# Kernel tuning notes

Hardware: AMD Instinct MI355X
Metric: run time of the kernel (lower is better)

## Reference

```python
import jax, jax.numpy as jnp
import numpy as np

ND, NT, B = 16384, 16384, 4096
FD, FT, C = 256, 256, 768


def _gat(x_src, x_dst, ei, Ws, Wd, a_s, a_d, b, num_dst, self_loops):
    """PyG GATConv, heads=1: per-edge attention softmax over incoming edges."""
    if self_loops:
        loops = jnp.arange(num_dst, dtype=ei.dtype)
        ei = jnp.concatenate([ei, jnp.stack([loops, loops])], axis=1)
    src, dst = ei[0], ei[1]
    hs = x_src @ Ws                                   # [Ns, C]
    hd = x_dst @ Wd                                   # [Ndst, C]
    e = jax.nn.leaky_relu((hs @ a_s)[src] + (hd @ a_d)[dst], 0.2)   # [E]
    m = jax.ops.segment_max(e, dst, num_segments=num_dst)
    p = jnp.exp(e - m[dst])
    s = jax.ops.segment_sum(p, dst, num_segments=num_dst)
    alpha = p / (s[dst] + 1e-16)
    out = jax.ops.segment_sum(hs[src] * alpha[:, None], dst, num_segments=num_dst)
    return out + b


def _l2norm(x):
    n = jnp.linalg.norm(x, axis=1, keepdims=True)
    return x / jnp.maximum(n, 1e-12)


def setup_inputs() -> dict:
    ks = iter(jax.random.split(jax.random.key(0), 64))
    def nrm(shape, fan_in=None):
        s = 1.0 if fan_in is None else (1.0 / fan_in) ** 0.5
        return jax.random.normal(next(ks), shape, jnp.float32) * s
    inp = {}
    inp["x_drug"] = nrm((ND, FD))
    inp["x_target"] = nrm((NT, FT))
    inp["cell_features"] = nrm((B, 890))
    for et, fs, fd in (("dd", FD, FD), ("dt", FD, FT), ("tt", FT, FT)):
        inp[f"W_src_{et}"] = nrm((fs, C), fs)
        inp[f"W_dst_{et}"] = nrm((fd, C), fd)
        inp[f"a_src_{et}"] = nrm((C,), C)
        inp[f"a_dst_{et}"] = nrm((C,), C)
        inp[f"b_{et}"] = jnp.zeros((C,), jnp.float32)
    for name, fi, fo in (("red1", 890, 2048), ("red2", 2048, 512), ("red3", 512, 2 * C),
                         ("r2a", 4 * C, 2048), ("r2b", 2048, 512), ("r2c", 512, C), ("cls", C, 2)):
        inp[f"{name}_w"] = nrm((fi, fo), fi)
        inp[f"{name}_b"] = jnp.zeros((fo,), jnp.float32)
    inp["drug1_id"] = jax.random.randint(next(ks), (B,), 0, ND)
    inp["drug2_id"] = jax.random.randint(next(ks), (B,), 0, ND)
    inp["ei_dd"] = jax.random.randint(next(ks), (2, 131072), 0, ND)
    inp["ei_dt"] = jnp.stack([jax.random.randint(next(ks), (262144,), 0, ND),
                              jax.random.randint(next(ks), (262144,), 0, NT)])
    inp["ei_tt"] = jax.random.randint(next(ks), (2, 262144), 0, NT)
    return inp


def reference(x_drug, x_target, cell_features,
              W_src_dd, W_dst_dd, a_src_dd, a_dst_dd, b_dd,
              W_src_dt, W_dst_dt, a_src_dt, a_dst_dt, b_dt,
              W_src_tt, W_dst_tt, a_src_tt, a_dst_tt, b_tt,
              red1_w, red1_b, red2_w, red2_b, red3_w, red3_b,
              r2a_w, r2a_b, r2b_w, r2b_b, r2c_w, r2c_b,
              cls_w, cls_b,
              drug1_id, drug2_id, ei_dd, ei_dt, ei_tt):
    # HeteroConv (aggr='sum') followed by per-type ReLU, num_layers=1
    drug = jax.nn.relu(_gat(x_drug, x_drug, ei_dd,
                            W_src_dd, W_dst_dd, a_src_dd, a_dst_dd, b_dd, ND, True))
    target = jax.nn.relu(
        _gat(x_drug, x_target, ei_dt, W_src_dt, W_dst_dt, a_src_dt, a_dst_dt, b_dt, NT, False)
        + _gat(x_target, x_target, ei_tt, W_src_tt, W_dst_tt, a_src_tt, a_dst_tt, b_tt, NT, True))
    del target  # with num_layers=1 the target embeddings never feed the output (faithful)
    d1 = drug[drug1_id]
    d2 = drug[drug2_id]
    cell = _l2norm(cell_features)
    cell = jax.nn.relu(cell @ red1_w + red1_b)
    cell = jax.nn.relu(cell @ red2_w + red2_b)
    cell = jax.nn.relu(cell @ red3_w + red3_b)          # [B, 2*C]
    hidden = _l2norm(jnp.concatenate([d1, d2, cell], axis=1))  # [B, 4*C]
    hidden = jax.nn.relu(hidden @ r2a_w + r2a_b)
    hidden = jax.nn.relu(hidden @ r2b_w + r2b_b)
    hidden = jax.nn.relu(hidden @ r2c_w + r2c_b)
    return hidden @ cls_w + cls_b                       # [B, 2]
```

## Files before the change

### kernel.cpp

```cpp
#include <hip/hip_runtime.h>
#include <cstdint>

#define ND 16384
#define BATCH 4096
#define CDIM 768
#define E_DD 131072
#define FD 256

typedef unsigned short u16;
typedef u16 u16x4 __attribute__((ext_vector_type(4)));
typedef u16 u16x8 __attribute__((ext_vector_type(8)));
typedef short s16x8 __attribute__((ext_vector_type(8)));
typedef float f32x4 __attribute__((ext_vector_type(4)));

__device__ __forceinline__ u16 f2bf(float x) {
  union { float f; uint32_t u; } v; v.f = x;
  uint32_t r = v.u + 0x7fffu + ((v.u >> 16) & 1u);
  return (u16)(r >> 16);
}
__device__ __forceinline__ float bf2f(u16 h) {
  union { float f; uint32_t u; } v; v.u = ((uint32_t)h) << 16;
  return v.f;
}
__device__ __forceinline__ uint32_t split2p(float x) {
  u16 h = f2bf(x);
  u16 l = f2bf(x - bf2f(h));
  return ((uint32_t)h << 16) | l;
}

#define GLOAD_LDS16(gp, lp)                                                   \
  __builtin_amdgcn_global_load_lds(                                           \
      (__attribute__((address_space(1))) void*)(gp),                          \
      (__attribute__((address_space(3))) void*)(lp), 16, 0, 0)

#define KP 40

template <int KS, int OUT_BF16, int RELU, int BIAS, int ASPLIT, int ALO, int BLO,
          int BKD>
__device__ __forceinline__ void gemm_core(
    int bx, int by, int bz,
    const float* __restrict__ Af,
    const u16* __restrict__ Ahi, const u16* __restrict__ Alo,
    const u16* __restrict__ Bhi, const u16* __restrict__ Blo,
    const float* __restrict__ bias,
    float* __restrict__ Cf, u16* __restrict__ Chi,
    int M, int N, int K, u16* AsB, u16* BsB) {
  constexpr int MT = 4, NT = 4;
  constexpr int BM = 128, BN = 128;
  constexpr int ASEG = BM / 64;
  constexpr int BSEG = BN / 64;
  constexpr bool DIRECT = (ASPLIT == 0 && ALO == 0 && BLO == 0);

  const int t = threadIdx.x;
  const int bm0 = bx * BM, bn0 = by * BN;
  const int wid = t >> 6, lane = t & 63;
  const int quad = lane >> 4, l16 = lane & 15;
  const int wm0 = (wid >> 1) * (MT * 16);
  const int wn0 = (wid & 1) * (NT * 16);

  const int chunk = K / KS;
  const int kbeg = (KS > 1) ? bz * chunk : 0;
  const int kend = kbeg + chunk;

  float bvv[NT];
#pragma unroll
  for (int ni = 0; ni < NT; ++ni)
    bvv[ni] = BIAS ? bias[bn0 + wn0 + ni * 16 + l16] : 0.f;

  f32x4 acc[MT][NT];
#pragma unroll
  for (int i = 0; i < MT; ++i)
#pragma unroll
    for (int j = 0; j < NT; ++j) acc[i][j] = (f32x4){0.f, 0.f, 0.f, 0.f};

  if constexpr (DIRECT) {
    constexpr int SLOTS = BKD / 8;
    constexpr int SM = SLOTS - 1;
    constexpr int NLD = (BM * BKD) / (256 * 8);
    auto stageA = [&](int buf, int kk) {
#pragma unroll
      for (int c = 0; c < NLD; ++c) {
        int s = t + 256 * c;
        int r = s / SLOTS, j = s % SLOTS;
        int jj = j ^ (r & SM);
        size_t goff = (size_t)(bm0 + r) * K + kk + jj * 8;
        int lofs = __builtin_amdgcn_readfirstlane((wid * 64 + 256 * c) * 8);
        GLOAD_LDS16(Ahi + goff, AsB + buf * (BM * BKD) + lofs);
      }
    };
    auto stageB = [&](int buf, int kk) {
#pragma unroll
      for (int c = 0; c < NLD; ++c) {
        int s = t + 256 * c;
        int r = s / SLOTS, j = s % SLOTS;
        int jj = j ^ (r & SM);
        size_t goff = (size_t)(bn0 + r) * K + kk + jj * 8;
        int lofs = __builtin_amdgcn_readfirstlane((wid * 64 + 256 * c) * 8);
        GLOAD_LDS16(Bhi + goff, BsB + buf * (BN * BKD) + lofs);
      }
    };
    const int rsw = l16 & SM;
    stageA(0, kbeg);
    stageB(0, kbeg);
    int cur = 0;
    for (int k0 = kbeg;;) {
      __syncthreads();
      int kn = k0 + BKD;
      if (kn < kend) {
        stageA(cur ^ 1, kn);
        stageB(cur ^ 1, kn);
      }
      const u16* Ab = AsB + cur * (BM * BKD);
      const u16* Bb = BsB + cur * (BN * BKD);
#pragma unroll
      for (int h = 0; h < BKD / 32; ++h) {
        s16x8 ah[MT], bh[NT];
#pragma unroll
        for (int mi = 0; mi < MT; ++mi)
          ah[mi] = *(const s16x8*)(Ab + (wm0 + mi * 16 + l16) * BKD +
                                   (((h * 4 + quad) ^ rsw) * 8));
#pragma unroll
        for (int ni = 0; ni < NT; ++ni)
          bh[ni] = *(const s16x8*)(Bb + (wn0 + ni * 16 + l16) * BKD +
                                   (((h * 4 + quad) ^ rsw) * 8));
#pragma unroll
        for (int mi = 0; mi < MT; ++mi)
#pragma unroll
          for (int ni = 0; ni < NT; ++ni)
            acc[mi][ni] = __builtin_amdgcn_mfma_f32_16x16x32_bf16(
                ah[mi], bh[ni], acc[mi][ni], 0, 0, 0);
      }
      k0 = kn;
      cur ^= 1;
      if (k0 >= kend) break;
    }
  } else {
    auto As = [&](int a, int r, int k) -> u16& { return AsB[(a * BM + r) * KP + k]; };
    auto Bs = [&](int a, int r, int k) -> u16& { return BsB[(a * BN + r) * KP + k]; };

    u16x8 pAh[ASEG], pAl[ASEG], pBh[BSEG], pBl[BSEG];

    auto loadA = [&](int c, int kk) {
      int s = t + 256 * c, row = s >> 2, kq = (s & 3) * 8;
      size_t off = (size_t)(bm0 + row) * K + kk + kq;
      if (ASPLIT) {
        f32x4 v0 = *(const f32x4*)(Af + off);
        f32x4 v1 = *(const f32x4*)(Af + off + 4);
        u16x8 h, l;
#pragma unroll
        for (int e = 0; e < 4; ++e) {
          uint32_t p = split2p(v0[e]);
          h[e] = (u16)(p >> 16); l[e] = (u16)(p & 0xffffu);
          uint32_t q = split2p(v1[e]);
          h[e + 4] = (u16)(q >> 16); l[e + 4] = (u16)(q & 0xffffu);
        }
        pAh[c] = h; pAl[c] = l;
      } else {
        pAh[c] = *(const u16x8*)(Ahi + off);
        if (ALO) pAl[c] = *(const u16x8*)(Alo + off);
      }
    };
    auto loadB = [&](int c, int kk) {
      int s = t + 256 * c, row = s >> 2, kq = (s & 3) * 8;
      size_t off = (size_t)(bn0 + row) * K + kk + kq;
      pBh[c] = *(const u16x8*)(Bhi + off);
      if (BLO) pBl[c] = *(const u16x8*)(Blo + off);
    };

#pragma unroll
    for (int c = 0; c < ASEG; ++c) loadA(c, kbeg);
#pragma unroll
    for (int c = 0; c < BSEG; ++c) loadB(c, kbeg);

    for (int k0 = kbeg;;) {
      __syncthreads();
#pragma unroll
      for (int c = 0; c < ASEG; ++c) {
        int s = t + 256 * c, row = s >> 2, kq = (s & 3) * 8;
        *(u16x8*)&As(0, row, kq) = pAh[c];
        if (ALO) *(u16x8*)&As(1, row, kq) = pAl[c];
      }
#pragma unroll
      for (int c = 0; c < BSEG; ++c) {
        int s = t + 256 * c, row = s >> 2, kq = (s & 3) * 8;
        *(u16x8*)&Bs(0, row, kq) = pBh[c];
        if (BLO) *(u16x8*)&Bs(1, row, kq) = pBl[c];
      }
      __syncthreads();

      int kn = k0 + 32;
      if (kn < kend) {
#pragma unroll
        for (int c = 0; c < ASEG; ++c) loadA(c, kn);
#pragma unroll
        for (int c = 0; c < BSEG; ++c) loadB(c, kn);
      }

      s16x8 ah[MT], al[MT], bh[NT], bl[NT];
#pragma unroll
      for (int mi = 0; mi < MT; ++mi) {
        ah[mi] = *(const s16x8*)&As(0, wm0 + mi * 16 + l16, quad * 8);
        if (ALO) al[mi] = *(const s16x8*)&As(1, wm0 + mi * 16 + l16, quad * 8);
      }
#pragma unroll
      for (int ni = 0; ni < NT; ++ni) {
        bh[ni] = *(const s16x8*)&Bs(0, wn0 + ni * 16 + l16, quad * 8);
        if (BLO) bl[ni] = *(const s16x8*)&Bs(1, wn0 + ni * 16 + l16, quad * 8);
      }
#pragma unroll
      for (int mi = 0; mi < MT; ++mi)
#pragma unroll
        for (int ni = 0; ni < NT; ++ni) {
          acc[mi][ni] = __builtin_amdgcn_mfma_f32_16x16x32_bf16(
              ah[mi], bh[ni], acc[mi][ni], 0, 0, 0);
          if (BLO)
            acc[mi][ni] = __builtin_amdgcn_mfma_f32_16x16x32_bf16(
                ah[mi], bl[ni], acc[mi][ni], 0, 0, 0);
          if (ALO)
            acc[mi][ni] = __builtin_amdgcn_mfma_f32_16x16x32_bf16(
                al[mi], bh[ni], acc[mi][ni], 0, 0, 0);
        }
      k0 = kn;
      if (k0 >= kend) break;
    }
  }

  float* Cp = (KS > 1) ? Cf + (size_t)bz * M * N : Cf;
#pragma unroll
  for (int mi = 0; mi < MT; ++mi) {
#pragma unroll
    for (int ni = 0; ni < NT; ++ni) {
      int row = bm0 + wm0 + mi * 16 + quad * 4;
      int col = bn0 + wn0 + ni * 16 + l16;
#pragma unroll
      for (int r = 0; r < 4; ++r) {
        float v = acc[mi][ni][r] + bvv[ni];
        if (RELU) v = fmaxf(v, 0.f);
        size_t o = (size_t)(row + r) * N + col;
        if (OUT_BF16) Chi[o] = f2bf(v);
        else Cp[o] = v;
      }
    }
  }
}

template <int KS, int OUT_BF16, int RELU, int BIAS, int ASPLIT, int ALO, int BLO,
          int BKD>
__global__ __launch_bounds__(256) void mfma_gemm(
    const float* __restrict__ Af,
    const u16* __restrict__ Ahi, const u16* __restrict__ Alo,
    const u16* __restrict__ Bhi, const u16* __restrict__ Blo,
    const float* __restrict__ bias,
    float* __restrict__ Cf, u16* __restrict__ Chi,
    int M, int N, int K) {
  constexpr bool DIRECT = (ASPLIT == 0 && ALO == 0 && BLO == 0);
  __shared__ __align__(16) u16 AsB[DIRECT ? 2 * 128 * BKD : (ALO ? 2 : 1) * 128 * KP];
  __shared__ __align__(16) u16 BsB[DIRECT ? 2 * 128 * BKD : (BLO ? 2 : 1) * 128 * KP];
  gemm_core<KS, OUT_BF16, RELU, BIAS, ASPLIT, ALO, BLO, BKD>(
      blockIdx.x, blockIdx.y, (KS > 1) ? (int)blockIdx.z : 0,
      Af, Ahi, Alo, Bhi, Blo, bias, Cf, Chi, M, N, K, AsB, BsB);
}

__device__ __forceinline__ void gat_body(
    int idx, int t,
    const u16* __restrict__ hs, const float* __restrict__ es,
    const float* __restrict__ ed, const int* __restrict__ offsets,
    const int* __restrict__ slots, const float* __restrict__ bias,
    const int* __restrict__ list, const int* __restrict__ cnt,
    u16* __restrict__ out) {
  if (idx >= *cnt) return;
  int d = list[idx];
  int lane = t & 63;
  int beg = offsets[d], end = offsets[d + 1];
  float edv = ed[d];
  float mx = -1e30f;
  for (int j = beg + lane; j < end; j += 64) {
    float e = es[slots[j]] + edv;
    e = e >= 0.f ? e : 0.2f * e;
    mx = fmaxf(mx, e);
  }
#pragma unroll
  for (int m = 32; m; m >>= 1) mx = fmaxf(mx, __shfl_xor(mx, m));
  float sm = 0.f;
  for (int j = beg + lane; j < end; j += 64) {
    float e = es[slots[j]] + edv;
    e = e >= 0.f ? e : 0.2f * e;
    sm += expf(e - mx);
  }
#pragma unroll
  for (int m = 32; m; m >>= 1) sm += __shfl_xor(sm, m);
  float inv = 1.f / (sm + 1e-16f);
  int c8 = lane * 8;
  int c4 = 512 + lane * 4;
  float a8[8] = {};
  float a4[4] = {};
  for (int j = beg; j < end; ++j) {
    int srcn = slots[j];
    float e = es[srcn] + edv;
    e = e >= 0.f ? e : 0.2f * e;
    float alpha = expf(e - mx) * inv;
    const u16* hrow = hs + (size_t)srcn * CDIM;
    u16x8 r8 = *(const u16x8*)(hrow + c8);
    u16x4 r4 = *(const u16x4*)(hrow + c4);
#pragma unroll
    for (int e2 = 0; e2 < 8; ++e2) a8[e2] = fmaf(alpha, bf2f(r8[e2]), a8[e2]);
#pragma unroll
    for (int e2 = 0; e2 < 4; ++e2) a4[e2] = fmaf(alpha, bf2f(r4[e2]), a4[e2]);
  }
  u16* orow = out + (size_t)d * CDIM;
  u16x8 o8;
  u16x4 o4;
#pragma unroll
  for (int e2 = 0; e2 < 8; ++e2) o8[e2] = f2bf(fmaxf(a8[e2] + bias[c8 + e2], 0.f));
#pragma unroll
  for (int e2 = 0; e2 < 4; ++e2) o4[e2] = f2bf(fmaxf(a4[e2] + bias[c4 + e2], 0.f));
  *(u16x8*)(orow + c8) = o8;
  *(u16x4*)(orow + c4) = o4;
}

__global__ __launch_bounds__(256) void dual_gemm_red1_hs_scatter(
    const u16* __restrict__ cn, const u16* __restrict__ r1T,
    const float* __restrict__ red1_b, u16* __restrict__ c1,
    const float* __restrict__ xd, const u16* __restrict__ wsrcT,
    u16* __restrict__ hs,
    const int* __restrict__ src, const int* __restrict__ dst,
    int* __restrict__ cursor, int* __restrict__ slots) {
  __shared__ __align__(16) u16 SMEM[16384];
  int b = blockIdx.x;
  if (b < 512) {
    gemm_core<1, 1, 1, 1, 0, 0, 0, 32>(b & 31, b >> 5, 0, nullptr, cn, nullptr,
                                       r1T, nullptr, red1_b, nullptr, c1,
                                       BATCH, 2048, 896, SMEM, SMEM + 2 * 128 * 32);
  } else if (b < 1280) {
    int b2 = b - 512;
    gemm_core<1, 1, 0, 0, 1, 1, 0, 32>(b2 & 127, b2 >> 7, 0, xd, nullptr, nullptr,
                                       wsrcT, nullptr, nullptr, nullptr, hs,
                                       ND, CDIM, FD, SMEM, SMEM + 2 * 128 * KP);
  } else {
    int e = (b - 1280) * 256 + threadIdx.x;
    if (e < E_DD) {
      int pos = atomicAdd(&cursor[dst[e]], 1);
      slots[pos] = src[e];
    }
  }
}

__global__ __launch_bounds__(256) void red2_gat(
    const u16* __restrict__ c1, const u16* __restrict__ r2T,
    float* __restrict__ P,
    const u16* __restrict__ hs, const float* __restrict__ es,
    const float* __restrict__ ed, const int* __restrict__ offsets,
    const int* __restrict__ slots, const float* __restrict__ bias,
    const int* __restrict__ list, const int* __restrict__ cnt,
    u16* __restrict__ drug) {
  __shared__ __align__(16) u16 SMEM[16384];
  int b = blockIdx.x;
  if (b < 512) {
    gemm_core<4, 0, 0, 0, 0, 0, 0, 32>(b & 31, (b >> 5) & 3, b >> 7,
                                       nullptr, c1, nullptr, r2T, nullptr,
                                       nullptr, P, nullptr,
                                       BATCH, 512, 2048, SMEM, SMEM + 2 * 128 * 32);
  } else {
    gat_body((b - 512) * 4 + (threadIdx.x >> 6), threadIdx.x,
             hs, es, ed, offsets, slots, bias, list, cnt, drug);
  }
}

template <int KS>
__global__ void reduce_split_ks(const float* __restrict__ P,
                                const float* __restrict__ bias,
                                u16* __restrict__ Chi, int M, int N) {
  int i = blockIdx.x * 256 + threadIdx.x;
  int total = (M * N) >> 2;
  if (i >= total) return;
  f32x4 s = ((const f32x4*)P)[i];
#pragma unroll
  for (int z = 1; z < KS; ++z) s += ((const f32x4*)P)[(size_t)z * total + i];
  int col = (i * 4) % N;
  f32x4 bv = *(const f32x4*)(bias + col);
  u16x4 h;
#pragma unroll
  for (int e = 0; e < 4; ++e) h[e] = f2bf(fmaxf(s[e] + bv[e], 0.f));
  *(u16x4*)&Chi[i * 4] = h;
}

__global__ void reduce_cls(const float* __restrict__ P,
                           const float* __restrict__ bias,
                           const float* __restrict__ clsw,
                           const float* __restrict__ clsb,
                           float* __restrict__ out) {
  int row = blockIdx.x * 4 + (threadIdx.x >> 6);
  int lane = threadIdx.x & 63;
  const f32x4* p0 = (const f32x4*)(P + (size_t)row * CDIM);
  const f32x4* p1 = (const f32x4*)(P + (size_t)BATCH * CDIM + (size_t)row * CDIM);
  float s0 = 0.f, s1 = 0.f;
#pragma unroll
  for (int i = 0; i < 3; ++i) {
    int c4 = lane + 64 * i;
    f32x4 a = p0[c4] + p1[c4];
    f32x4 bv = *(const f32x4*)(bias + c4 * 4);
#pragma unroll
    for (int e = 0; e < 4; ++e) {
      float h = fmaxf(a[e] + bv[e], 0.f);
      int c = c4 * 4 + e;
      s0 = fmaf(h, clsw[c * 2 + 0], s0);
      s1 = fmaf(h, clsw[c * 2 + 1], s1);
    }
  }
#pragma unroll
  for (int m = 32; m; m >>= 1) {
    s0 += __shfl_xor(s0, m);
    s1 += __shfl_xor(s1, m);
  }
  if (lane == 0) {
    out[row * 2 + 0] = s0 + clsb[0];
    out[row * 2 + 1] = s1 + clsb[1];
  }
}

struct TDesc {
  const float* W;
  u16* Th;
  int K, N, Kpad, start;
};
struct TPack { TDesc d[7]; };

#define P1_T 11328
#define P1_W (P1_T + 256)
#define P1_I (P1_W + 64)
__global__ __launch_bounds__(256) void prep1(
    TPack p,
    const float* __restrict__ Wsrc, const float* __restrict__ Wdst,
    const float* __restrict__ a_s, const float* __restrict__ a_d,
    float* __restrict__ wsv, float* __restrict__ wdv,
    int* __restrict__ counts, int* __restrict__ mask, int* __restrict__ cnt,
    const float* __restrict__ cellf, u16* __restrict__ cn_hi) {
  __shared__ __align__(16) float S[1088];
  int b = blockIdx.x;
  int t = threadIdx.x;
  if (b < P1_T) {
    float (*tile)[33] = (float(*)[33])S;
    int mi = 0;
#pragma unroll
    for (int i = 1; i < 7; ++i)
      if (b >= p.d[i].start) mi = i;
    TDesc dd = p.d[mi];
    int rel = b - dd.start;
    int tilesX = dd.Kpad / 32;
    int k0 = (rel % tilesX) * 32, n0 = (rel / tilesX) * 32;
    int tx = t & 31, ty = t >> 5;
#pragma unroll
    for (int i = 0; i < 4; ++i) {
      int k = k0 + ty + 8 * i, n = n0 + tx;
      tile[ty + 8 * i][tx] = (k < dd.K && n < dd.N) ? dd.W[(size_t)k * dd.N + n] : 0.f;
    }
    __syncthreads();
#pragma unroll
    for (int i = 0; i < 4; ++i) {
      int n = n0 + ty + 8 * i, k = k0 + tx;
      if (n < dd.N) dd.Th[(size_t)n * dd.Kpad + k] = f2bf(tile[tx][ty + 8 * i]);
    }
  } else if (b < P1_W) {
    int k = b - P1_T;
    float* rs = S;
    float* rd = S + 256;
    float s = 0.f, d = 0.f;
    for (int c = t; c < CDIM; c += 256) {
      s += Wsrc[(size_t)k * CDIM + c] * a_s[c];
      d += Wdst[(size_t)k * CDIM + c] * a_d[c];
    }
    rs[t] = s; rd[t] = d;
    __syncthreads();
    for (int st = 128; st; st >>= 1) {
      if (t < st) { rs[t] += rs[t + st]; rd[t] += rd[t + st]; }
      __syncthreads();
    }
    if (t == 0) { wsv[k] = rs[0]; wdv[k] = rd[0]; }
  } else if (b < P1_I) {
    int i = (b - P1_W) * 256 + t;
    if (i < ND) { counts[i] = 1; mask[i] = 0; }
    if (i == 0) *cnt = 0;
  } else {
    int row = b - P1_I;
    float* red = S;
    const float* irow = cellf + (size_t)row * 890;
    float s = 0.f;
    for (int c = t; c < 890; c += 256) { float v = irow[c]; s += v * v; }
    red[t] = s;
    __syncthreads();
    for (int st = 128; st; st >>= 1) {
      if (t < st) red[t] += red[t + st];
      __syncthreads();
    }
    float inv = 1.f / fmaxf(sqrtf(red[0]), 1e-12f);
    for (int c = t; c < 896; c += 256) {
      float v = (c < 890) ? irow[c] * inv : 0.f;
      cn_hi[(size_t)row * 896 + c] = f2bf(v);
    }
  }
}

#define P2_E (ND * FD / 1024)
#define P2_M (P2_E + BATCH / 256)
__global__ __launch_bounds__(256) void prep2(
    const float* __restrict__ x, const float* __restrict__ wsv,
    const float* __restrict__ wdv, float* __restrict__ es, float* __restrict__ ed,
    const int* __restrict__ d1, const int* __restrict__ d2, int* __restrict__ mask,
    const int* __restrict__ dst, int* __restrict__ counts) {
  int b = blockIdx.x, t = threadIdx.x;
  if (b < P2_E) {
    int i = b * 256 + t;
    int lane = t & 63;
    int row = i >> 6;
    int c4 = lane * 4;
    f32x4 v = ((const f32x4*)x)[i];
    f32x4 ws = *(const f32x4*)(wsv + c4);
    f32x4 wd = *(const f32x4*)(wdv + c4);
    float a = v[0] * ws[0] + v[1] * ws[1] + v[2] * ws[2] + v[3] * ws[3];
    float bb = v[0] * wd[0] + v[1] * wd[1] + v[2] * wd[2] + v[3] * wd[3];
#pragma unroll
    for (int m = 32; m; m >>= 1) {
      a += __shfl_xor(a, m);
      bb += __shfl_xor(bb, m);
    }
    if (lane == 0) { es[row] = a; ed[row] = bb; }
  } else if (b < P2_M) {
    int i = (b - P2_E) * 256 + t;
    mask[d1[i]] = 1;
    mask[d2[i]] = 1;
  } else {
    int e = (b - P2_M) * 256 + t;
    atomicAdd(&counts[dst[e]], 1);
  }
}

__global__ __launch_bounds__(512) void prep3(
    const int* __restrict__ mask, int* __restrict__ cnt, int* __restrict__ list,
    const int* __restrict__ counts, int* __restrict__ offsets,
    int* __restrict__ cursor, int* __restrict__ slots) {
  __shared__ int part[512];
  int b = blockIdx.x, t = threadIdx.x;
  if (b < 32) {
    int i = b * 512 + t;
    if (mask[i]) {
      int pos = atomicAdd(cnt, 1);
      list[pos] = i;
    }
  } else {
    int base = t * 32;
    int s = 0;
    for (int i = 0; i < 32; ++i) s += counts[base + i];
    part[t] = s;
    __syncthreads();
    if (t == 0) {
      int run = 0;
      for (int i = 0; i < 512; ++i) { int tmp = part[i]; part[i] = run; run += tmp; }
      offsets[ND] = run;
    }
    __syncthreads();
    int run = part[t];
    for (int i = 0; i < 32; ++i) {
      int d = base + i;
      offsets[d] = run;
      slots[run] = d;
      cursor[d] = run + 1;
      run += counts[d];
    }
  }
}

__global__ __launch_bounds__(256) void hidden_build_bf16(
    const u16* __restrict__ drug, const u16* __restrict__ c3,
    const int* __restrict__ d1, const int* __restrict__ d2,
    u16* __restrict__ hhi) {
  int row = blockIdx.x;
  int t = threadIdx.x;
  const u16* s1 = drug + (size_t)d1[row] * CDIM;
  const u16* s2 = drug + (size_t)d2[row] * CDIM;
  const u16* s3 = c3 + (size_t)row * (2 * CDIM);
  float vals[12];
  float ss = 0.f;
#pragma unroll
  for (int i = 0; i < 12; ++i) {
    int c = t + 256 * i;
    float v;
    if (i < 3)      v = bf2f(s1[c]);
    else if (i < 6) v = bf2f(s2[c - CDIM]);
    else            v = bf2f(s3[c - 2 * CDIM]);
    vals[i] = v;
    ss += v * v;
  }
  __shared__ float red[256];
  red[t] = ss;
  __syncthreads();
  for (int st = 128; st; st >>= 1) {
    if (t < st) red[t] += red[t + st];
    __syncthreads();
  }
  float inv = 1.f / fmaxf(sqrtf(red[0]), 1e-12f);
  u16* hrow_h = hhi + (size_t)row * (4 * CDIM);
#pragma unroll
  for (int i = 0; i < 12; ++i) hrow_h[t + 256 * i] = f2bf(vals[i] * inv);
}

extern "C" void kernel_launch(void* const* d_in, const int* in_sizes, int n_in,
                              void* d_out, int out_size, void* d_ws, size_t ws_size,
                              hipStream_t stream) {
  const float* x_drug   = (const float*)d_in[0];
  const float* cellf    = (const float*)d_in[2];
  const float* W_src_dd = (const float*)d_in[3];
  const float* W_dst_dd = (const float*)d_in[4];
  const float* a_src_dd = (const float*)d_in[5];
  const float* a_dst_dd = (const float*)d_in[6];
  const float* b_dd     = (const float*)d_in[7];
  const float* red1_w = (const float*)d_in[18];
  const float* red1_b = (const float*)d_in[19];
  const float* red2_w = (const float*)d_in[20];
  const float* red2_b = (const float*)d_in[21];
  const float* red3_w = (const float*)d_in[22];
  const float* red3_b = (const float*)d_in[23];
  const float* r2a_w  = (const float*)d_in[24];
  const float* r2a_b  = (const float*)d_in[25];
  const float* r2b_w  = (const float*)d_in[26];
  const float* r2b_b  = (const float*)d_in[27];
  const float* r2c_w  = (const float*)d_in[28];
  const float* r2c_b  = (const float*)d_in[29];
  const float* cls_w  = (const float*)d_in[30];
  const float* cls_b  = (const float*)d_in[31];
  const int* drug1_id = (const int*)d_in[32];
  const int* drug2_id = (const int*)d_in[33];
  const int* ei_dd    = (const int*)d_in[34];
  float* out = (float*)d_out;

  const int* dd_src = ei_dd;
  const int* dd_dst = ei_dd + E_DD;

  char* w = (char*)d_ws;
  size_t off = 0;
  auto alloc = [&](size_t bytes) -> char* {
    char* p = w + off;
    off = (off + bytes + 255) & ~(size_t)255;
    return p;
  };
  u16* hs   = (u16*)alloc((size_t)ND * CDIM * 2);
  u16* drug = (u16*)alloc((size_t)ND * CDIM * 2);
  u16* c3   = (u16*)alloc((size_t)BATCH * 2 * CDIM * 2);
  float* P  = (float*)alloc((size_t)4 * BATCH * 512 * 4);
  u16* hid_hi = hs;
  u16* cn_hi = (u16*)alloc((size_t)BATCH * 896 * 2);
  u16* c1_hi = (u16*)alloc((size_t)BATCH * 2048 * 2);
  u16* c2_hi = (u16*)alloc((size_t)BATCH * 512 * 2);
  u16* wsrcT_hi = (u16*)alloc((size_t)CDIM * FD * 2);
  u16* r1T_hi = (u16*)alloc((size_t)2048 * 896 * 2);
  u16* r2T_hi = (u16*)alloc((size_t)512 * 2048 * 2);
  u16* r3T_hi = (u16*)alloc((size_t)1536 * 512 * 2);
  u16* raT_hi = (u16*)alloc((size_t)2048 * 3072 * 2);
  u16* rbT_hi = (u16*)alloc((size_t)512 * 2048 * 2);
  u16* rcT_hi = (u16*)alloc((size_t)768 * 512 * 2);
  float* es  = (float*)alloc((size_t)ND * 4);
  float* ed  = (float*)alloc((size_t)ND * 4);
  float* wsv = (float*)alloc(FD * 4);
  float* wdv = (float*)alloc(FD * 4);
  int* counts  = (int*)alloc((size_t)ND * 4);
  int* offsets = (int*)alloc((size_t)(ND + 1) * 4);
  int* cursor  = (int*)alloc((size_t)ND * 4);
  int* slots   = (int*)alloc((size_t)(E_DD + ND) * 4);
  int* mask    = (int*)alloc((size_t)ND * 4);
  int* list    = (int*)alloc((size_t)ND * 4);
  int* cnt     = (int*)alloc(256);
  (void)ws_size; (void)n_in; (void)in_sizes; (void)out_size;

  TPack tp;
  tp.d[0] = {W_src_dd, wsrcT_hi, 256, 768, 256, 0};
  tp.d[1] = {red1_w, r1T_hi, 890, 2048, 896, 192};
  tp.d[2] = {red2_w, r2T_hi, 2048, 512, 2048, 1984};
  tp.d[3] = {red3_w, r3T_hi, 512, 1536, 512, 3008};
  tp.d[4] = {r2a_w, raT_hi, 3072, 2048, 3072, 3776};
  tp.d[5] = {r2b_w, rbT_hi, 2048, 512, 2048, 9920};
  tp.d[6] = {r2c_w, rcT_hi, 512, 768, 512, 10944};
  prep1<<<15744, 256, 0, stream>>>(tp, W_src_dd, W_dst_dd, a_src_dd, a_dst_dd,
                                   wsv, wdv, counts, mask, cnt, cellf, cn_hi);

  prep2<<<4624, 256, 0, stream>>>(x_drug, wsv, wdv, es, ed, drug1_id, drug2_id,
                                  mask, dd_dst, counts);

  prep3<<<33, 512, 0, stream>>>(mask, cnt, list, counts, offsets, cursor, slots);

  dual_gemm_red1_hs_scatter<<<1792, 256, 0, stream>>>(
      cn_hi, r1T_hi, red1_b, c1_hi, x_drug, wsrcT_hi, hs,
      dd_src, dd_dst, cursor, slots);

  red2_gat<<<4608, 256, 0, stream>>>(c1_hi, r2T_hi, P,
                                     hs, es, ed, offsets, slots, b_dd, list,
                                     cnt, drug);
  reduce_split_ks<4><<<BATCH * 512 / 1024, 256, 0, stream>>>(P, red2_b, c2_hi, BATCH, 512);
  mfma_gemm<1, 1, 1, 1, 0, 0, 0, 64><<<dim3(BATCH / 128, 1536 / 128), 256, 0, stream>>>(
      nullptr, c2_hi, nullptr, r3T_hi, nullptr, red3_b, nullptr, c3, BATCH, 1536, 512);

  hidden_build_bf16<<<BATCH, 256, 0, stream>>>(drug, c3, drug1_id, drug2_id, hid_hi);

  mfma_gemm<1, 1, 1, 1, 0, 0, 0, 64><<<dim3(BATCH / 128, 2048 / 128), 256, 0, stream>>>(
      nullptr, hid_hi, nullptr, raT_hi, nullptr, r2a_b, nullptr, c1_hi, BATCH, 2048, 3072);
  mfma_gemm<4, 0, 0, 0, 0, 0, 0, 64><<<dim3(BATCH / 128, 512 / 128, 4), 256, 0, stream>>>(
      nullptr, c1_hi, nullptr, rbT_hi, nullptr, nullptr, P, nullptr, BATCH, 512, 2048);
  reduce_split_ks<4><<<BATCH * 512 / 1024, 256, 0, stream>>>(P, r2b_b, c2_hi, BATCH, 512);
  mfma_gemm<2, 0, 0, 0, 0, 0, 0, 64><<<dim3(BATCH / 128, CDIM / 128, 2), 256, 0, stream>>>(
      nullptr, c2_hi, nullptr, rcT_hi, nullptr, nullptr, P, nullptr, BATCH, CDIM, 512);
  reduce_cls<<<BATCH / 4, 256, 0, stream>>>(P, r2c_b, cls_w, cls_b, out);
}
```

Before: 445.0 us.

## Remap GEMM workgroups per XCD and split red2 GEMM from GAT aggregation

Result: no change. 452.3 us (+1.6%).

```diff
diff --git a/kernel.cpp b/kernel.cpp
--- a/kernel.cpp
+++ b/kernel.cpp
@@ -32,6 +32,12 @@
   __builtin_amdgcn_global_load_lds(                                           \
       (__attribute__((address_space(1))) void*)(gp),                          \
       (__attribute__((address_space(3))) void*)(lp), 16, 0, 0)
+
+__device__ __forceinline__ int xcd_chunk(int f, int nwg) {
+  int q = nwg >> 3, r = nwg & 7;
+  int xcd = f & 7, s = f >> 3;
+  return (xcd < r ? xcd * (q + 1) : r * (q + 1) + (xcd - r) * q) + s;
+}
 
 #define KP 40
 
@@ -256,8 +262,11 @@
   constexpr bool DIRECT = (ASPLIT == 0 && ALO == 0 && BLO == 0);
   __shared__ __align__(16) u16 AsB[DIRECT ? 2 * 128 * BKD : (ALO ? 2 : 1) * 128 * KP];
   __shared__ __align__(16) u16 BsB[DIRECT ? 2 * 128 * BKD : (BLO ? 2 : 1) * 128 * KP];
+  int f = blockIdx.x + gridDim.x * blockIdx.y;
+  int wg = xcd_chunk(f, gridDim.x * gridDim.y);
+  int bx = wg % gridDim.x, by = wg / gridDim.x;
   gemm_core<KS, OUT_BF16, RELU, BIAS, ASPLIT, ALO, BLO, BKD>(
-      blockIdx.x, blockIdx.y, (KS > 1) ? (int)blockIdx.z : 0,
+      bx, by, (KS > 1) ? (int)blockIdx.z : 0,
       Af, Ahi, Alo, Bhi, Blo, bias, Cf, Chi, M, N, K, AsB, BsB);
 }
 
@@ -318,6 +327,16 @@
   *(u16x4*)(orow + c4) = o4;
 }
 
+__global__ __launch_bounds__(256) void gat_aggregate(
+    const u16* __restrict__ hs, const float* __restrict__ es,
+    const float* __restrict__ ed, const int* __restrict__ offsets,
+    const int* __restrict__ slots, const float* __restrict__ bias,
+    const int* __restrict__ list, const int* __restrict__ cnt,
+    u16* __restrict__ out) {
+  gat_body(blockIdx.x * 4 + (threadIdx.x >> 6), threadIdx.x,
+           hs, es, ed, offsets, slots, bias, list, cnt, out);
+}
+
 __global__ __launch_bounds__(256) void dual_gemm_red1_hs_scatter(
     const u16* __restrict__ cn, const u16* __restrict__ r1T,
     const float* __restrict__ red1_b, u16* __restrict__ c1,
@@ -328,7 +347,8 @@
   __shared__ __align__(16) u16 SMEM[16384];
   int b = blockIdx.x;
   if (b < 512) {
-    gemm_core<1, 1, 1, 1, 0, 0, 0, 32>(b & 31, b >> 5, 0, nullptr, cn, nullptr,
+    int wg = xcd_chunk(b, 512);
+    gemm_core<1, 1, 1, 1, 0, 0, 0, 32>(wg & 31, wg >> 5, 0, nullptr, cn, nullptr,
                                        r1T, nullptr, red1_b, nullptr, c1,
                                        BATCH, 2048, 896, SMEM, SMEM + 2 * 128 * 32);
   } else if (b < 1280) {
@@ -342,27 +362,6 @@
       int pos = atomicAdd(&cursor[dst[e]], 1);
       slots[pos] = src[e];
     }
-  }
-}
-
-__global__ __launch_bounds__(256) void red2_gat(
-    const u16* __restrict__ c1, const u16* __restrict__ r2T,
-    float* __restrict__ P,
-    const u16* __restrict__ hs, const float* __restrict__ es,
-    const float* __restrict__ ed, const int* __restrict__ offsets,
-    const int* __restrict__ slots, const float* __restrict__ bias,
-    const int* __restrict__ list, const int* __restrict__ cnt,
-    u16* __restrict__ drug) {
-  __shared__ __align__(16) u16 SMEM[16384];
-  int b = blockIdx.x;
-  if (b < 512) {
-    gemm_core<4, 0, 0, 0, 0, 0, 0, 32>(b & 31, (b >> 5) & 3, b >> 7,
-                                       nullptr, c1, nullptr, r2T, nullptr,
-                                       nullptr, P, nullptr,
-                                       BATCH, 512, 2048, SMEM, SMEM + 2 * 128 * 32);
-  } else {
-    gat_body((b - 512) * 4 + (threadIdx.x >> 6), threadIdx.x,
-             hs, es, ed, offsets, slots, bias, list, cnt, drug);
   }
 }
 
@@ -690,12 +689,13 @@
       cn_hi, r1T_hi, red1_b, c1_hi, x_drug, wsrcT_hi, hs,
       dd_src, dd_dst, cursor, slots);
 
-  red2_gat<<<4608, 256, 0, stream>>>(c1_hi, r2T_hi, P,
-                                     hs, es, ed, offsets, slots, b_dd, list,
-                                     cnt, drug);
+  mfma_gemm<4, 0, 0, 0, 0, 0, 0, 64><<<dim3(BATCH / 128, 512 / 128, 4), 256, 0, stream>>>(
+      nullptr, c1_hi, nullptr, r2T_hi, nullptr, nullptr, P, nullptr, BATCH, 512, 2048);
   reduce_split_ks<4><<<BATCH * 512 / 1024, 256, 0, stream>>>(P, red2_b, c2_hi, BATCH, 512);
   mfma_gemm<1, 1, 1, 1, 0, 0, 0, 64><<<dim3(BATCH / 128, 1536 / 128), 256, 0, stream>>>(
       nullptr, c2_hi, nullptr, r3T_hi, nullptr, red3_b, nullptr, c3, BATCH, 1536, 512);
+
+  gat_aggregate<<<ND / 4, 256, 0, stream>>>(hs, es, ed, offsets, slots, b_dd, list, cnt, drug);
 
   hidden_build_bf16<<<BATCH, 256, 0, stream>>>(drug, c3, drug1_id, drug2_id, hid_hi);
 
```
